# Optimization experiments

Measured on AMD Instinct MI355X. Metric: run time of the kernel, lower is better.

Reference implementation:

```python
import jax, jax.numpy as jnp
import numpy as np


def setup_inputs() -> dict:
    key = jax.random.key(0)
    k1, k2 = jax.random.split(key)
    B, C, L, K = 16, 64, 4096, 1024
    x = jax.random.normal(k1, (B, C, L), dtype=jnp.float32)
    codebook = jax.random.normal(k2, (K, C), dtype=jnp.float32)
    return {"x": x, "codebook": codebook}


def reference(x, codebook):
    # x: (B, C, L), codebook: (K, C)
    B, C, L = x.shape
    xt = jnp.transpose(x, (0, 2, 1))  # (B, L, C)

    # Squared Euclidean distances (argmin is invariant to the sqrt in torch.cdist)
    x2 = jnp.sum(xt * xt, axis=-1, keepdims=True)            # (B, L, 1)
    w2 = jnp.sum(codebook * codebook, axis=-1)               # (K,)
    xw = jnp.einsum("blc,kc->blk", xt, codebook)             # (B, L, K)
    d2 = x2 - 2.0 * xw + w2                                   # (B, L, K)
    min_encoding_indices = jnp.argmin(d2, axis=-1)            # (B, L)

    quant = codebook[min_encoding_indices]                    # (B, L, C)

    commitment_loss = jnp.mean((jax.lax.stop_gradient(quant) - xt) ** 2)
    codebook_loss = jnp.mean((quant - jax.lax.stop_gradient(xt)) ** 2)

    # Straight-through estimator
    quant_out = xt + jax.lax.stop_gradient(quant - xt)        # (B, L, C)
    quant_out = jnp.transpose(quant_out, (0, 2, 1))           # (B, C, L)

    return quant_out, codebook_loss, commitment_loss, min_encoding_indices
```

## Files before the change

kernel.cpp:

```cpp
#include <hip/hip_runtime.h>

#define BATCH 16
#define CH    64
#define LEN   4096
#define NCODE 1024
#define NPTS  (BATCH * LEN)
#define NPART 512
#define UNITB 24576

typedef float float2v __attribute__((ext_vector_type(2)));
typedef float float4v __attribute__((ext_vector_type(4)));
typedef short short8  __attribute__((ext_vector_type(8)));
typedef float f32x16  __attribute__((ext_vector_type(16)));
typedef unsigned int uint32;

__device__ __forceinline__ unsigned short f2bf(float f) {
    uint32 u = __builtin_bit_cast(uint32, f);
    u += 0x7fffu + ((u >> 16) & 1u);
    return (unsigned short)(u >> 16);
}
__device__ __forceinline__ float bf2f(unsigned short h) {
    uint32 u = ((uint32)h) << 16;
    return __builtin_bit_cast(float, u);
}

__global__ __launch_bounds__(256) void vq_prep(const float* __restrict__ cb,
                                               short* __restrict__ cbf2,
                                               float* __restrict__ w2tab) {
    int k = blockIdx.x * 256 + threadIdx.x;
    if (k >= NCODE) return;
    const int T = k >> 5, row = k & 31;
    const int Tp = (T < 16) ? (T * 2) : ((T - 16) * 2 + 1);
    float s2 = 0.f;
    for (int c = 0; c < CH; ++c) {
        float xv = cb[(size_t)k * CH + c];
        s2 = fmaf(xv, xv, s2);
        unsigned short h1 = f2bf(xv); float f1 = bf2f(h1);
        float r1 = xv - f1;
        unsigned short h2 = f2bf(r1); float f2 = bf2f(h2);
        float r2 = r1 - f2;
        unsigned short h3 = f2bf(r2);
        int s = c >> 4, kk = c & 15, g = kk >> 3, i = kk & 7;
        int lane = g * 32 + row;
        size_t base = ((size_t)Tp * 12 + s * 3) * 512 + lane * 8 + i;
        cbf2[base]        = (short)h1;
        cbf2[base + 512]  = (short)h2;
        cbf2[base + 1024] = (short)h3;
    }
    int hi = (row >> 2) & 1, r = (row & 3) + 4 * (row >> 3);
    w2tab[((size_t)T * 2 + hi) * 16 + r] = s2;
}

__device__ __forceinline__ void epi(const f32x16& acc, int Tg, int g,
                                    float& bestc, int& bestk,
                                    const float* w2s) {
    const float4v* wt = (const float4v*)(w2s + ((size_t)Tg * 2 + g) * 16);
    float4v w0 = wt[0], w1 = wt[1], w2v = wt[2], w3 = wt[3];
    float wr[16] = {w0.x, w0.y, w0.z, w0.w, w1.x, w1.y, w1.z, w1.w,
                    w2v.x, w2v.y, w2v.z, w2v.w, w3.x, w3.y, w3.z, w3.w};
    int kbase = Tg * 32 + 4 * g;
#pragma unroll
    for (int r = 0; r < 16; ++r) {
        float cost = fmaf(-2.0f, acc[r], wr[r]);
        int kg = kbase + (r & 3) + 8 * (r >> 2);
        if (cost < bestc) { bestc = cost; bestk = kg; }
    }
}

__global__ void __launch_bounds__(512)
__attribute__((amdgpu_waves_per_eu(4, 4)))
vq_argmin(const float*  __restrict__ x,
          const float*  __restrict__ cb,
          const short*  __restrict__ cbf2,
          const float*  __restrict__ w2tab,
          float*        __restrict__ quant,
          float*        __restrict__ idx_out,
          double*       __restrict__ partial) {
    __shared__ __attribute__((aligned(16))) char  ring[3 * UNITB];
    __shared__ __attribute__((aligned(16))) float w2s[NCODE];
    __shared__ float  smc[8][32];
    __shared__ int    smk[8][32];
    __shared__ int    fidx[128];
    __shared__ double sds[128];

    const int t   = threadIdx.x;
    const int l   = t & 63;
    const int w   = __builtin_amdgcn_readfirstlane(t >> 6);
    const int h2  = w >> 2;
    const int ptl = (w & 3) * 32 + (l & 31);
    const int g   = l >> 5;
    const int p0  = blockIdx.x * 128;
    const int b   = p0 >> 12;
    const int l0  = p0 & (LEN - 1);

    float* xs = (float*)ring;

#pragma unroll
    for (int it = 0; it < 4; ++it) {
        int fi = it * 512 + t, c = fi >> 5, p4 = fi & 31;
        *(float4v*)&xs[c * 128 + 4 * p4] =
            *(const float4v*)&x[((size_t)b * CH + c) * LEN + l0 + 4 * p4];
    }
    w2s[t]       = w2tab[t];
    w2s[t + 512] = w2tab[t + 512];
    __syncthreads();

    short8 B1[4], B2[4], B3[4];
    float x2p = 0.f;
#pragma unroll
    for (int s = 0; s < 4; ++s) {
#pragma unroll
        for (int i = 0; i < 8; ++i) {
            int c = s * 16 + g * 8 + i;
            float xv = xs[c * 128 + ptl];
            x2p = fmaf(xv, xv, x2p);
            unsigned short h1v = f2bf(xv); float f1 = bf2f(h1v);
            float r1 = xv - f1;
            unsigned short h2v = f2bf(r1); float f2 = bf2f(h2v);
            float r2 = r1 - f2;
            unsigned short h3v = f2bf(r2);
            B1[s][i] = (short)h1v; B2[s][i] = (short)h2v; B3[s][i] = (short)h3v;
        }
    }
    const float x2 = x2p + __shfl_xor(x2p, 32, 64);
    __syncthreads();

    const float4v* gsrc = (const float4v*)cbf2;

    float4v sA0, sA1, sA2, sB0, sB1, sB2;
    sA0 = gsrc[t]; sA1 = gsrc[512 + t]; sA2 = gsrc[1024 + t];
    {
        float4v* d = (float4v*)ring;
        d[t] = sA0; d[512 + t] = sA1; d[1024 + t] = sA2;
    }
    sA0 = gsrc[1536 + t]; sA1 = gsrc[2048 + t]; sA2 = gsrc[2560 + t];
    asm volatile("" ::: "memory");
    __builtin_amdgcn_s_barrier();
    asm volatile("" ::: "memory");

    float bestc = 3.4e38f;
    int   bestk = 0;

    auto STEP = [&](int tt, float4v& cu0, float4v& cu1, float4v& cu2,
                    float4v& nx0, float4v& nx1, float4v& nx2) {
        if (tt + 2 < 16) {
            const float4v* gs = gsrc + (size_t)(tt + 2) * 1536;
            nx0 = gs[t]; nx1 = gs[512 + t]; nx2 = gs[1024 + t];
        }
        const short* bp = (const short*)&ring[(tt % 3) * UNITB] + h2 * 6144;
        f32x16 acc = {0.f,0.f,0.f,0.f,0.f,0.f,0.f,0.f,
                      0.f,0.f,0.f,0.f,0.f,0.f,0.f,0.f};
#pragma unroll
        for (int s = 0; s < 4; ++s) {
            const short* fb = bp + (s * 3) * 512 + l * 8;
            short8 A1 = *(const short8*)(fb);
            short8 A2 = *(const short8*)(fb + 512);
            short8 A3 = *(const short8*)(fb + 1024);
            acc = __builtin_amdgcn_mfma_f32_32x32x16_bf16(A1, B1[s], acc, 0, 0, 0);
            acc = __builtin_amdgcn_mfma_f32_32x32x16_bf16(A1, B2[s], acc, 0, 0, 0);
            acc = __builtin_amdgcn_mfma_f32_32x32x16_bf16(A2, B1[s], acc, 0, 0, 0);
            acc = __builtin_amdgcn_mfma_f32_32x32x16_bf16(A1, B3[s], acc, 0, 0, 0);
            acc = __builtin_amdgcn_mfma_f32_32x32x16_bf16(A3, B1[s], acc, 0, 0, 0);
            acc = __builtin_amdgcn_mfma_f32_32x32x16_bf16(A2, B2[s], acc, 0, 0, 0);
        }
        epi(acc, h2 * 16 + tt, g, bestc, bestk, w2s);
        if (tt + 1 < 16) {
            float4v* d = (float4v*)&ring[((tt + 1) % 3) * UNITB];
            d[t] = cu0; d[512 + t] = cu1; d[1024 + t] = cu2;
        }
        asm volatile("" ::: "memory");
        __builtin_amdgcn_s_barrier();
        asm volatile("" ::: "memory");
    };

    for (int tp = 0; tp < 8; ++tp) {
        STEP(2 * tp,     sA0, sA1, sA2, sB0, sB1, sB2);
        STEP(2 * tp + 1, sB0, sB1, sB2, sA0, sA1, sA2);
    }

    {
        float ob = __shfl_xor(bestc, 32, 64);
        int   ok = __shfl_xor(bestk, 32, 64);
        if (ob < bestc || (ob == bestc && ok < bestk)) { bestc = ob; bestk = ok; }
    }
    if (l < 32) { smc[w][l] = bestc; smk[w][l] = bestk; }
    __syncthreads();
    if (w < 4 && l < 32) {
        float ob = smc[w + 4][l];
        int   ok = smk[w + 4][l];
        if (ob < bestc || (ob == bestc && ok < bestk)) { bestc = ob; bestk = ok; }
        idx_out[p0 + w * 32 + l] = (float)bestk;
        fidx[w * 32 + l] = bestk;
        sds[w * 32 + l] = (double)x2 + (double)bestc;
    }
    __syncthreads();

    {
        const int pt = t & 127;
        const int cq = t >> 7;
        const int k  = fidx[pt];
        const float4v* src = (const float4v*)(cb + (size_t)k * CH + cq * 16);
        float4v v0 = src[0], v1 = src[1], v2 = src[2], v3 = src[3];
        float vr[16] = {v0.x, v0.y, v0.z, v0.w, v1.x, v1.y, v1.z, v1.w,
                        v2.x, v2.y, v2.z, v2.w, v3.x, v3.y, v3.z, v3.w};
#pragma unroll
        for (int j = 0; j < 16; ++j) {
            int c = cq * 16 + j;
            quant[((size_t)b * CH + c) * LEN + l0 + pt] = vr[j];
        }
    }

    if (t == 0) {
        double s = 0.0;
        for (int i = 0; i < 128; ++i) s += sds[i];
        partial[blockIdx.x] = s;
    }
}

__global__ __launch_bounds__(256) void vq_loss(const double* __restrict__ partial,
                                               float*        __restrict__ losses) {
    __shared__ double sred[256];
    double v = 0.0;
#pragma unroll
    for (int i = 0; i < NPART / 256; ++i) v += partial[threadIdx.x + 256 * i];
    sred[threadIdx.x] = v;
    __syncthreads();
    for (int s = 128; s > 0; s >>= 1) {
        if (threadIdx.x < s) sred[threadIdx.x] += sred[threadIdx.x + s];
        __syncthreads();
    }
    if (threadIdx.x == 0) {
        float loss = (float)(sred[0] / (double)((size_t)NPTS * CH));
        losses[0] = loss;
        losses[1] = loss;
    }
}

extern "C" void kernel_launch(void* const* d_in, const int* in_sizes, int n_in,
                              void* d_out, int out_size, void* d_ws, size_t ws_size,
                              hipStream_t stream) {
    const float* x  = (const float*)d_in[0];
    const float* cb = (const float*)d_in[1];
    float* out = (float*)d_out;

    float* quant_out = out;
    float* losses    = out + (size_t)BATCH * CH * LEN;
    float* idx_out   = losses + 2;

    double* partial = (double*)d_ws;
    float*  w2tab   = (float*)((char*)d_ws + 4096);
    short*  cbf2    = (short*)((char*)d_ws + 16384);

    vq_prep<<<NCODE / 256, 256, 0, stream>>>(cb, cbf2, w2tab);
    vq_argmin<<<NPTS / 128, 512, 0, stream>>>(x, cb, cbf2, w2tab,
                                              quant_out, idx_out, partial);
    vq_loss<<<1, 256, 0, stream>>>(partial, losses);
}
```

Baseline: 72.41 us.

## Parallelize codebook prep, double-buffer the LDS ring, split MFMA accumulator chains

```diff
diff --git a/kernel.cpp b/kernel.cpp
--- a/kernel.cpp
+++ b/kernel.cpp
@@ -27,28 +27,47 @@
 __global__ __launch_bounds__(256) void vq_prep(const float* __restrict__ cb,
                                                short* __restrict__ cbf2,
                                                float* __restrict__ w2tab) {
-    int k = blockIdx.x * 256 + threadIdx.x;
-    if (k >= NCODE) return;
-    const int T = k >> 5, row = k & 31;
+    __shared__ float tile[64][65];
+    __shared__ float s2p[4][64];
+    const int k0 = blockIdx.x * 64;
+    const int t  = threadIdx.x;
+#pragma unroll
+    for (int it = 0; it < 4; ++it) {
+        int idx = it * 256 + t, row = idx >> 4, q = idx & 15;
+        *(float4v*)&tile[row][q * 4] =
+            *(const float4v*)&cb[(size_t)(k0 + row) * CH + q * 4];
+    }
+    __syncthreads();
+
+    const int j  = t & 63;
+    const int cq = t >> 6;
+    const int k  = k0 + j, T = k >> 5, row = k & 31;
     const int Tp = (T < 16) ? (T * 2) : ((T - 16) * 2 + 1);
     float s2 = 0.f;
-    for (int c = 0; c < CH; ++c) {
-        float xv = cb[(size_t)k * CH + c];
+#pragma unroll
+    for (int cc = 0; cc < 16; ++cc) {
+        float xv = tile[j][cq * 16 + cc];
         s2 = fmaf(xv, xv, s2);
         unsigned short h1 = f2bf(xv); float f1 = bf2f(h1);
         float r1 = xv - f1;
         unsigned short h2 = f2bf(r1); float f2 = bf2f(h2);
         float r2 = r1 - f2;
         unsigned short h3 = f2bf(r2);
-        int s = c >> 4, kk = c & 15, g = kk >> 3, i = kk & 7;
+        int g = cc >> 3, i = cc & 7;
         int lane = g * 32 + row;
-        size_t base = ((size_t)Tp * 12 + s * 3) * 512 + lane * 8 + i;
+        size_t base = ((size_t)Tp * 12 + cq * 3) * 512 + lane * 8 + i;
         cbf2[base]        = (short)h1;
         cbf2[base + 512]  = (short)h2;
         cbf2[base + 1024] = (short)h3;
     }
-    int hi = (row >> 2) & 1, r = (row & 3) + 4 * (row >> 3);
-    w2tab[((size_t)T * 2 + hi) * 16 + r] = s2;
+    s2p[cq][j] = s2;
+    __syncthreads();
+    if (t < 64) {
+        float s2t = ((s2p[0][t] + s2p[1][t]) + (s2p[2][t] + s2p[3][t]));
+        int kk = k0 + t, TT = kk >> 5, rr = kk & 31;
+        int hi = (rr >> 2) & 1, r = (rr & 3) + 4 * (rr >> 3);
+        w2tab[((size_t)TT * 2 + hi) * 16 + r] = s2t;
+    }
 }
 
 __device__ __forceinline__ void epi(const f32x16& acc, int Tg, int g,
@@ -76,7 +95,7 @@
           float*        __restrict__ quant,
           float*        __restrict__ idx_out,
           double*       __restrict__ partial) {
-    __shared__ __attribute__((aligned(16))) char  ring[3 * UNITB];
+    __shared__ __attribute__((aligned(16))) char  ring[2 * UNITB];
     __shared__ __attribute__((aligned(16))) float w2s[NCODE];
     __shared__ float  smc[8][32];
     __shared__ int    smk[8][32];
@@ -134,7 +153,7 @@
         d[t] = sA0; d[512 + t] = sA1; d[1024 + t] = sA2;
     }
     sA0 = gsrc[1536 + t]; sA1 = gsrc[2048 + t]; sA2 = gsrc[2560 + t];
-    asm volatile("" ::: "memory");
+    asm volatile("s_waitcnt lgkmcnt(0)" ::: "memory");
     __builtin_amdgcn_s_barrier();
     asm volatile("" ::: "memory");
 
@@ -147,28 +166,30 @@
             const float4v* gs = gsrc + (size_t)(tt + 2) * 1536;
             nx0 = gs[t]; nx1 = gs[512 + t]; nx2 = gs[1024 + t];
         }
-        const short* bp = (const short*)&ring[(tt % 3) * UNITB] + h2 * 6144;
-        f32x16 acc = {0.f,0.f,0.f,0.f,0.f,0.f,0.f,0.f,
-                      0.f,0.f,0.f,0.f,0.f,0.f,0.f,0.f};
+        const short* bp = (const short*)&ring[(tt & 1) * UNITB] + h2 * 6144;
+        f32x16 acc1 = {0.f,0.f,0.f,0.f,0.f,0.f,0.f,0.f,
+                       0.f,0.f,0.f,0.f,0.f,0.f,0.f,0.f};
+        f32x16 acc2 = acc1;
 #pragma unroll
         for (int s = 0; s < 4; ++s) {
             const short* fb = bp + (s * 3) * 512 + l * 8;
             short8 A1 = *(const short8*)(fb);
             short8 A2 = *(const short8*)(fb + 512);
             short8 A3 = *(const short8*)(fb + 1024);
-            acc = __builtin_amdgcn_mfma_f32_32x32x16_bf16(A1, B1[s], acc, 0, 0, 0);
-            acc = __builtin_amdgcn_mfma_f32_32x32x16_bf16(A1, B2[s], acc, 0, 0, 0);
-            acc = __builtin_amdgcn_mfma_f32_32x32x16_bf16(A2, B1[s], acc, 0, 0, 0);
-            acc = __builtin_amdgcn_mfma_f32_32x32x16_bf16(A1, B3[s], acc, 0, 0, 0);
-            acc = __builtin_amdgcn_mfma_f32_32x32x16_bf16(A3, B1[s], acc, 0, 0, 0);
-            acc = __builtin_amdgcn_mfma_f32_32x32x16_bf16(A2, B2[s], acc, 0, 0, 0);
-        }
+            acc1 = __builtin_amdgcn_mfma_f32_32x32x16_bf16(A1, B1[s], acc1, 0, 0, 0);
+            acc2 = __builtin_amdgcn_mfma_f32_32x32x16_bf16(A1, B2[s], acc2, 0, 0, 0);
+            acc1 = __builtin_amdgcn_mfma_f32_32x32x16_bf16(A2, B1[s], acc1, 0, 0, 0);
+            acc2 = __builtin_amdgcn_mfma_f32_32x32x16_bf16(A1, B3[s], acc2, 0, 0, 0);
+            acc1 = __builtin_amdgcn_mfma_f32_32x32x16_bf16(A3, B1[s], acc1, 0, 0, 0);
+            acc2 = __builtin_amdgcn_mfma_f32_32x32x16_bf16(A2, B2[s], acc2, 0, 0, 0);
+        }
+        f32x16 acc = acc1 + acc2;
         epi(acc, h2 * 16 + tt, g, bestc, bestk, w2s);
         if (tt + 1 < 16) {
-            float4v* d = (float4v*)&ring[((tt + 1) % 3) * UNITB];
+            float4v* d = (float4v*)&ring[((tt + 1) & 1) * UNITB];
             d[t] = cu0; d[512 + t] = cu1; d[1024 + t] = cu2;
         }
-        asm volatile("" ::: "memory");
+        asm volatile("s_waitcnt lgkmcnt(0)" ::: "memory");
         __builtin_amdgcn_s_barrier();
         asm volatile("" ::: "memory");
     };
@@ -251,7 +272,7 @@
     float*  w2tab   = (float*)((char*)d_ws + 4096);
     short*  cbf2    = (short*)((char*)d_ws + 16384);
 
-    vq_prep<<<NCODE / 256, 256, 0, stream>>>(cb, cbf2, w2tab);
+    vq_prep<<<16, 256, 0, stream>>>(cb, cbf2, w2tab);
     vq_argmin<<<NPTS / 128, 512, 0, stream>>>(x, cb, cbf2, w2tab,
                                               quant_out, idx_out, partial);
     vq_loss<<<1, 256, 0, stream>>>(partial, losses);
```

New measurement: 70.87 us. 1.02x faster.
